# Kernel tuning notes

Measured on AMD Instinct MI355X. Metric: run time of the kernel, lower is better.

Reference implementation:

```python
import jax, jax.numpy as jnp
import numpy as np

D_MODEL = 1024
NUM_HEADS = 2
NUM_FEATURES = 256
DEPTH = D_MODEL // 2  # faithful to source: depth = d_model // 2
B, L = 4, 4096


def _orthogonal_gaussian(key, m, d):
    # Faithful port of orthogonal_gaussian: stacked QR blocks, scaled.
    num_squares = m // d
    remainder = m - d * num_squares
    keys = jax.random.split(key, num_squares + 1)
    blocks = []
    for i in range(num_squares):
        q, _ = jnp.linalg.qr(jax.random.normal(keys[i], (d, d)))
        blocks.append(q.T)
    if remainder:
        q, _ = jnp.linalg.qr(jax.random.normal(keys[-1], (d, d)))
        blocks.append(q.T[:remainder])
    mat = jnp.vstack(blocks)
    return mat / jnp.sqrt(jnp.float32(num_squares) + remainder / d)


def setup_inputs() -> dict:
    key = jax.random.key(0)
    ks = jax.random.split(key, 16)
    s = 0.02
    inp = {
        'query': jax.random.normal(ks[0], (B, L, D_MODEL), jnp.float32),
        'key':   jax.random.normal(ks[1], (B, L, D_MODEL), jnp.float32),
        'value': jax.random.normal(ks[2], (B, L, D_MODEL), jnp.float32),
        'mask':  jnp.zeros((B, 1, 1, L), jnp.float32),
        'Wq': jax.random.normal(ks[3], (D_MODEL, D_MODEL), jnp.float32) * s,
        'bq': jnp.zeros((D_MODEL,), jnp.float32),
        'Wk': jax.random.normal(ks[4], (D_MODEL, D_MODEL), jnp.float32) * s,
        'bk': jnp.zeros((D_MODEL,), jnp.float32),
        'Wv': jax.random.normal(ks[5], (D_MODEL, D_MODEL), jnp.float32) * s,
        'bv': jnp.zeros((D_MODEL,), jnp.float32),
        'Wo': jax.random.normal(ks[6], (D_MODEL, D_MODEL), jnp.float32) * s,
        'bo': jnp.zeros((D_MODEL,), jnp.float32),
        'random_feats': _orthogonal_gaussian(ks[7], NUM_FEATURES, DEPTH),
    }
    return inp


def _softmax_kernel(data, is_query, proj, eps=1e-6):
    # data: [B, L, H, D]; proj: [M, D]
    d = data.shape[-1]
    data = data * (1.0 / jnp.sqrt(jnp.sqrt(jnp.float32(d))))
    ratio = 1.0 / jnp.sqrt(jnp.float32(proj.shape[0]))
    data_dash = jnp.einsum('blhd,md->blhm', data, proj)  # [B,L,H,M]
    diag = jnp.sum(data * data, axis=-1, keepdims=True) * 0.5  # [B,L,H,1]
    if is_query:
        mx = jnp.max(data_dash, axis=-1, keepdims=True)
    else:
        # last_dims_t + attention_dims_t = (3, 1)
        mx = jnp.max(data_dash, axis=(3, 1), keepdims=True)
    return ratio * (jnp.exp(data_dash - diag - mx) + eps)


def _attn_hat(q, k, v, proj):
    # q,k,v: [B, H, Lh, D]  (Lh = 2L/num_heads from split_heads quirk)
    l = q.shape[0]  # faithful: tf.shape(query)[0] == batch
    q = jnp.transpose(q, (0, 2, 1, 3))  # [B, Lh, H, D]
    k = jnp.transpose(k, (0, 2, 1, 3))
    q_prime = _softmax_kernel(q, True, proj)   # [B, Lh, H, M]
    k_prime = _softmax_kernel(k, False, proj)
    v = jnp.transpose(v, (0, 2, 1, 3))         # [B, Lh, H, D]
    # Faithful einsums: axis0 labeled 'l' (=batch), axis1 labeled 'b' (=seq)
    av = jnp.einsum('lbhm,lbhd->bhmd', k_prime, v)
    av = jnp.einsum('lbhm,bhmd->lbhd', q_prime, av)
    norm = jnp.einsum('lbhm,l->bhm', k_prime, jnp.ones((l,), jnp.float32))
    norm = jnp.einsum('lbhm,bhm->lbh', q_prime, norm)
    av = jnp.transpose(av, (1, 0, 2, 3))       # [Lh, B, H, D]
    norm = jnp.transpose(norm, (1, 0, 2))[..., None]
    return av / norm


def reference(query, key, value, mask, Wq, bq, Wk, bk, Wv, bv, Wo, bo, random_feats):
    bsz = query.shape[0]
    q = query @ Wq + bq
    k = key @ Wk + bk
    v = value @ Wv + bv

    def split_heads(x):
        x = x.reshape(bsz, -1, NUM_HEADS, DEPTH)
        return jnp.transpose(x, (0, 2, 1, 3))

    q, k, v = split_heads(q), split_heads(k), split_heads(v)
    attn = _attn_hat(q, k, v, random_feats)        # [Lh, B, H, D]
    attn = jnp.transpose(attn, (0, 2, 1, 3))       # [Lh, H, B, D]
    concat = attn.reshape(bsz, -1, D_MODEL)
    return concat @ Wo + bo
```

## Files before the change

kernel.cpp:

```cpp
#include <hip/hip_runtime.h>
#include <cstdint>
#include <cstddef>

typedef unsigned short u16;
typedef __bf16 bf16x8 __attribute__((ext_vector_type(8)));
typedef unsigned short u16x8 __attribute__((ext_vector_type(8)));
typedef float   f32x4 __attribute__((ext_vector_type(4)));

#define D_MODEL 1024
#define NF      256
#define DEPTH   512
#define SEQ     4096
#define ROWS    16384
#define HROWS   32768

#define QK_SCALE      0.21022410381342864f
#define HALF_SCALE2   0.022097086912079608f

__device__ __forceinline__ u16 f2bf(float f) {
  union { float f; uint32_t u; } x; x.f = f;
  uint32_t r = x.u + 0x7FFFu + ((x.u >> 16) & 1u);
  return (u16)(r >> 16);
}
__device__ __forceinline__ float bf2f(u16 u) {
  union { uint32_t u; float f; } x; x.u = ((uint32_t)u) << 16;
  return x.f;
}

__device__ __forceinline__ void gload16(const u16* g, u16* l) {
  __builtin_amdgcn_global_load_lds((const __attribute__((address_space(1))) void*)g,
                                   (__attribute__((address_space(3))) void*)l,
                                   16, 0, 0);
}


__global__ void transpose4_kernel(const float* __restrict__ w0, const float* __restrict__ w1,
                                  const float* __restrict__ w2, const float* __restrict__ w3,
                                  u16* __restrict__ o0, u16* __restrict__ o1,
                                  u16* __restrict__ o2, u16* __restrict__ o3) {
  __shared__ float tile[32][33];
  int z = blockIdx.z;
  const float* src = (z == 0) ? w0 : (z == 1) ? w1 : (z == 2) ? w2 : w3;
  u16* dst         = (z == 0) ? o0 : (z == 1) ? o1 : (z == 2) ? o2 : o3;
  int bx = blockIdx.x * 32, by = blockIdx.y * 32;
  int tx = threadIdx.x, ty = threadIdx.y;
#pragma unroll
  for (int r = ty; r < 32; r += 8) tile[r][tx] = src[(size_t)(by + r) * D_MODEL + bx + tx];
  __syncthreads();
#pragma unroll
  for (int r = ty; r < 32; r += 8)
    dst[(size_t)(bx + r) * D_MODEL + by + tx] = f2bf(tile[tx][r]);
}

__global__ void projcvt_kernel(const float4* __restrict__ p, ushort4* __restrict__ o) {
  int i = blockIdx.x * 256 + threadIdx.x;
  float4 a = p[i];
  o[i] = make_ushort4(f2bf(a.x * QK_SCALE), f2bf(a.y * QK_SCALE),
                      f2bf(a.z * QK_SCALE), f2bf(a.w * QK_SCALE));
}

template <bool BF16OUT, bool AFP32>
__global__ __launch_bounds__(256) void gemm_bt_kernel(
    const void* __restrict__ Av, const u16* __restrict__ B, void* __restrict__ Cv,
    const float* __restrict__ bias, int K, int N) {
  __shared__ __align__(16) u16 As[128 * 32];
  __shared__ __align__(16) u16 Bs[128 * 32];
  const int tid  = threadIdx.x;
  const int lane = tid & 63;
  const int wave = tid >> 6;
  const int wm = wave >> 1, wn = wave & 1;
  const int quad = lane >> 4, l15 = lane & 15;
  const int bm = blockIdx.x, bn = blockIdx.y;
  const u16* Bb = (const u16*)B + (size_t)bn * 128 * K;

  const int srow = lane >> 2;
  const int scol = (lane & 3) * 8;
  const u16* Bg0 = Bb + (size_t)(wave * 32 + srow) * K + scol;
  const u16* Bg1 = Bg0 + (size_t)16 * K;
  u16* lA0 = As + wave * 1024;
  u16* lA1 = lA0 + 512;
  u16* lB0 = Bs + wave * 1024;
  u16* lB1 = lB0 + 512;

  const u16*   Ag0  = nullptr; const u16*   Ag1  = nullptr;
  const float* Af0  = nullptr; const float* Af1  = nullptr;
  if (AFP32) {
    const float* Ab = (const float*)Av + (size_t)bm * 128 * K;
    Af0 = Ab + (size_t)(wave * 32 + srow) * K + scol;
    Af1 = Af0 + (size_t)16 * K;
  } else {
    const u16* Ab = (const u16*)Av + (size_t)bm * 128 * K;
    Ag0 = Ab + (size_t)(wave * 32 + srow) * K + scol;
    Ag1 = Ag0 + (size_t)16 * K;
  }
  u16* wA0 = As + wave * 1024 + lane * 8;
  u16* wA1 = wA0 + 512;

  f32x4 acc[4][4] = {};

  for (int k0 = 0; k0 < K; k0 += 32) {
    __syncthreads();
    if (AFP32) {
      float4 p00 = *(const float4*)(Af0 + k0);
      float4 p01 = *(const float4*)(Af0 + k0 + 4);
      float4 p10 = *(const float4*)(Af1 + k0);
      float4 p11 = *(const float4*)(Af1 + k0 + 4);
      gload16(Bg0 + k0, lB0);
      gload16(Bg1 + k0, lB1);
      u16x8 c0, c1;
      c0[0]=f2bf(p00.x); c0[1]=f2bf(p00.y); c0[2]=f2bf(p00.z); c0[3]=f2bf(p00.w);
      c0[4]=f2bf(p01.x); c0[5]=f2bf(p01.y); c0[6]=f2bf(p01.z); c0[7]=f2bf(p01.w);
      c1[0]=f2bf(p10.x); c1[1]=f2bf(p10.y); c1[2]=f2bf(p10.z); c1[3]=f2bf(p10.w);
      c1[4]=f2bf(p11.x); c1[5]=f2bf(p11.y); c1[6]=f2bf(p11.z); c1[7]=f2bf(p11.w);
      *(u16x8*)wA0 = c0;
      *(u16x8*)wA1 = c1;
    } else {
      gload16(Ag0 + k0, lA0);
      gload16(Ag1 + k0, lA1);
      gload16(Bg0 + k0, lB0);
      gload16(Bg1 + k0, lB1);
    }
    __syncthreads();
    bf16x8 af[4], bfr[4];
#pragma unroll
    for (int mt = 0; mt < 4; mt++)
      af[mt] = *(const bf16x8*)&As[(wm * 64 + mt * 16 + l15) * 32 + quad * 8];
#pragma unroll
    for (int nt = 0; nt < 4; nt++)
      bfr[nt] = *(const bf16x8*)&Bs[(wn * 64 + nt * 16 + l15) * 32 + quad * 8];
#pragma unroll
    for (int mt = 0; mt < 4; mt++)
#pragma unroll
      for (int nt = 0; nt < 4; nt++)
        acc[mt][nt] = __builtin_amdgcn_mfma_f32_16x16x32_bf16(af[mt], bfr[nt], acc[mt][nt], 0, 0, 0);
  }

  const int rbase = bm * 128 + wm * 64 + quad * 4;
  const int cbase = bn * 128 + wn * 64 + l15;
#pragma unroll
  for (int nt = 0; nt < 4; nt++) {
    int col = cbase + nt * 16;
    float bvad = bias ? bias[col] : 0.0f;
#pragma unroll
    for (int mt = 0; mt < 4; mt++) {
#pragma unroll
      for (int r = 0; r < 4; r++) {
        int row = rbase + mt * 16 + r;
        float v = acc[mt][nt][r] + bvad;
        if (BF16OUT) ((u16*)Cv)[(size_t)row * N + col] = f2bf(v);
        else         ((float*)Cv)[(size_t)row * N + col] = v;
      }
    }
  }
}

__global__ void diag_kernel(const u16* __restrict__ Qb, const u16* __restrict__ Kb,
                            float* __restrict__ dq, float* __restrict__ dk) {
  const int wave = threadIdx.x >> 6, lane = threadIdx.x & 63;
  int row = blockIdx.x * 4 + wave;
  const u16* src; float* dst; int r;
  if (row < HROWS) { src = Qb; dst = dq; r = row; }
  else             { src = Kb; dst = dk; r = row - HROWS; }
  const ushort4* p = (const ushort4*)(src + (size_t)r * DEPTH);
  ushort4 u0 = p[lane * 2], u1 = p[lane * 2 + 1];
  float s = 0.f, f;
  f = bf2f(u0.x); s += f * f; f = bf2f(u0.y); s += f * f;
  f = bf2f(u0.z); s += f * f; f = bf2f(u0.w); s += f * f;
  f = bf2f(u1.x); s += f * f; f = bf2f(u1.y); s += f * f;
  f = bf2f(u1.z); s += f * f; f = bf2f(u1.w); s += f * f;
#pragma unroll
  for (int o = 32; o; o >>= 1) s += __shfl_xor(s, o);
  if (lane == 0) dst[r] = s * HALF_SCALE2;
}

__global__ void maxk_part_kernel(const float* __restrict__ kd, float* __restrict__ partials) {
  int g = blockIdx.x >> 6;
  int sb = blockIdx.x & 63;
  int b = g >> 1, h = g & 1;
  int tid = threadIdx.x;
  float mx = -3.4e38f;
  for (int j = 0; j < 64; j++) {
    int s = sb * 64 + j;
    int row = b * 8192 + s * 2 + h;
    mx = fmaxf(mx, kd[(size_t)row * NF + tid]);
  }
#pragma unroll
  for (int o = 32; o; o >>= 1) mx = fmaxf(mx, __shfl_xor(mx, o));
  __shared__ float wmax[4];
  if ((tid & 63) == 0) wmax[tid >> 6] = mx;
  __syncthreads();
  if (tid == 0)
    partials[blockIdx.x] = fmaxf(fmaxf(wmax[0], wmax[1]), fmaxf(wmax[2], wmax[3]));
}

__global__ void maxk_final_kernel(const float* __restrict__ partials, float* __restrict__ mxk) {
  float v = partials[blockIdx.x * 64 + threadIdx.x];
#pragma unroll
  for (int o = 32; o; o >>= 1) v = fmaxf(v, __shfl_xor(v, o));
  if (threadIdx.x == 0) mxk[blockIdx.x] = v;
}

__global__ __launch_bounds__(256) void attn_kernel(
    const float* __restrict__ qd, const float* __restrict__ kd,
    const float* __restrict__ diagq, const float* __restrict__ diagk,
    const float* __restrict__ mxk, const u16* __restrict__ Vb,
    u16* __restrict__ concat) {
  int s = blockIdx.x >> 1, h = blockIdx.x & 1;
  int t = threadIdx.x;
  int wave = t >> 6, lane = t & 63;
  __shared__ float qp[4][256], kp[4][256];
  __shared__ float As[4][4];
  __shared__ float wred[4][4];
  __shared__ float mqs[4];

  float qv[4], kv[4];
  int rows[4];
#pragma unroll
  for (int b = 0; b < 4; b++) {
    int r = b * 8192 + s * 2 + h;
    rows[b] = r;
    qv[b] = qd[(size_t)r * NF + t];
    kv[b] = kd[(size_t)r * NF + t];
  }
#pragma unroll
  for (int b = 0; b < 4; b++) {
    float v = qv[b];
#pragma unroll
    for (int o = 32; o; o >>= 1) v = fmaxf(v, __shfl_xor(v, o));
    if (lane == 0) wred[wave][b] = v;
  }
  __syncthreads();
  if (t < 4) mqs[t] = fmaxf(fmaxf(wred[0][t], wred[1][t]), fmaxf(wred[2][t], wred[3][t]));
  __syncthreads();
#pragma unroll
  for (int b = 0; b < 4; b++) {
    qp[b][t] = __expf(qv[b] - diagq[rows[b]] - mqs[b]) + 1e-6f;
    kp[b][t] = __expf(kv[b] - diagk[rows[b]] - mxk[b * 2 + h]) + 1e-6f;
  }
  __syncthreads();
  {
    int i = wave;
    float p0 = 0, p1 = 0, p2 = 0, p3 = 0;
    for (int m = lane; m < 256; m += 64) {
      float q = qp[i][m];
      p0 += q * kp[0][m]; p1 += q * kp[1][m];
      p2 += q * kp[2][m]; p3 += q * kp[3][m];
    }
#pragma unroll
    for (int o = 32; o; o >>= 1) {
      p0 += __shfl_xor(p0, o); p1 += __shfl_xor(p1, o);
      p2 += __shfl_xor(p2, o); p3 += __shfl_xor(p3, o);
    }
    if (lane == 0) { As[i][0] = p0; As[i][1] = p1; As[i][2] = p2; As[i][3] = p3; }
  }
  __syncthreads();
  float a00 = As[0][0], a01 = As[0][1], a02 = As[0][2], a03 = As[0][3];
  float a10 = As[1][0], a11 = As[1][1], a12 = As[1][2], a13 = As[1][3];
  float a20 = As[2][0], a21 = As[2][1], a22 = As[2][2], a23 = As[2][3];
  float a30 = As[3][0], a31 = As[3][1], a32 = As[3][2], a33 = As[3][3];
  float n0 = 1.f / (a00 + a01 + a02 + a03);
  float n1 = 1.f / (a10 + a11 + a12 + a13);
  float n2 = 1.f / (a20 + a21 + a22 + a23);
  float n3 = 1.f / (a30 + a31 + a32 + a33);
  size_t obase = (size_t)s * 4096 + (size_t)h * 2048;
#pragma unroll
  for (int dp = 0; dp < 2; dp++) {
    int d = t + dp * 256;
    float v0 = bf2f(Vb[((size_t)(0 * SEQ + s)) * D_MODEL + h * DEPTH + d]);
    float v1 = bf2f(Vb[((size_t)(1 * SEQ + s)) * D_MODEL + h * DEPTH + d]);
    float v2 = bf2f(Vb[((size_t)(2 * SEQ + s)) * D_MODEL + h * DEPTH + d]);
    float v3 = bf2f(Vb[((size_t)(3 * SEQ + s)) * D_MODEL + h * DEPTH + d]);
    concat[obase + 0 * 512 + d] = f2bf((a00 * v0 + a01 * v1 + a02 * v2 + a03 * v3) * n0);
    concat[obase + 1 * 512 + d] = f2bf((a10 * v0 + a11 * v1 + a12 * v2 + a13 * v3) * n1);
    concat[obase + 2 * 512 + d] = f2bf((a20 * v0 + a21 * v1 + a22 * v2 + a23 * v3) * n2);
    concat[obase + 3 * 512 + d] = f2bf((a30 * v0 + a31 * v1 + a32 * v2 + a33 * v3) * n3);
  }
}

extern "C" void kernel_launch(void* const* d_in, const int* in_sizes, int n_in,
                              void* d_out, int out_size, void* d_ws, size_t ws_size,
                              hipStream_t stream) {
  (void)in_sizes; (void)n_in; (void)out_size; (void)ws_size;
  const float* query = (const float*)d_in[0];
  const float* key   = (const float*)d_in[1];
  const float* value = (const float*)d_in[2];
  const float* Wq = (const float*)d_in[4];
  const float* bq = (const float*)d_in[5];
  const float* Wk = (const float*)d_in[6];
  const float* bk = (const float*)d_in[7];
  const float* Wv = (const float*)d_in[8];
  const float* bv = (const float*)d_in[9];
  const float* Wo = (const float*)d_in[10];
  const float* bo = (const float*)d_in[11];
  const float* proj = (const float*)d_in[12];
  float* out = (float*)d_out;

  char* w = (char*)d_ws;
  size_t o = 0;
  auto take = [&](size_t b) { void* p = w + o; o += (b + 255) & ~(size_t)255; return p; };
  u16* Wqt   = (u16*)take(2097152);
  u16* Wkt   = (u16*)take(2097152);
  u16* Wvt   = (u16*)take(2097152);
  u16* Wot   = (u16*)take(2097152);
  u16* projb = (u16*)take(262144);
  u16* Qb    = (u16*)take(33554432);
  u16* Kb    = (u16*)take(33554432);
  u16* Vb    = (u16*)take(33554432);
  float* qd  = (float*)take(33554432);
  float* kd  = (float*)take(33554432);
  u16* concat = (u16*)take(33554432);
  float* diagq    = (float*)take(131072);
  float* diagk    = (float*)take(131072);
  float* partials = (float*)take(2048);
  float* mxk      = (float*)take(64);

  transpose4_kernel<<<dim3(32, 32, 4), dim3(32, 8), 0, stream>>>(Wq, Wk, Wv, Wo,
                                                                 Wqt, Wkt, Wvt, Wot);
  projcvt_kernel<<<128, 256, 0, stream>>>((const float4*)proj, (ushort4*)projb);

  gemm_bt_kernel<true, true><<<dim3(128, 8), 256, 0, stream>>>(query, Wqt, Qb, bq, 1024, 1024);
  gemm_bt_kernel<true, true><<<dim3(128, 8), 256, 0, stream>>>(key,   Wkt, Kb, bk, 1024, 1024);
  gemm_bt_kernel<true, true><<<dim3(128, 8), 256, 0, stream>>>(value, Wvt, Vb, bv, 1024, 1024);

  diag_kernel<<<16384, 256, 0, stream>>>(Qb, Kb, diagq, diagk);

  gemm_bt_kernel<false, false><<<dim3(256, 2), 256, 0, stream>>>(Qb, projb, qd, nullptr, 512, 256);
  gemm_bt_kernel<false, false><<<dim3(256, 2), 256, 0, stream>>>(Kb, projb, kd, nullptr, 512, 256);

  maxk_part_kernel<<<512, 256, 0, stream>>>(kd, partials);
  maxk_final_kernel<<<8, 64, 0, stream>>>(partials, mxk);

  attn_kernel<<<8192, 256, 0, stream>>>(qd, kd, diagq, diagk, mxk, Vb, concat);

  gemm_bt_kernel<false, false><<<dim3(128, 8), 256, 0, stream>>>(concat, Wot, out, bo, 1024, 1024);
}
```

Measured before the change: 621.2 us.

## Double-buffer GEMM LDS tiles and swizzle chunks to avoid bank conflicts

The bf16 GEMM now holds two LDS buffers for A and B. The loads for the next K-slice are issued before the MFMAs on the current slice, so global memory latency can overlap compute. The 8-element column chunks are also rotated per row on both the write and the read side to cut LDS bank conflicts on the fragment reads. This doubles LDS use per block, which may lower occupancy. It also depends on the async global-to-LDS loads having finished by the barrier at the top of the next iteration.

```diff
diff --git a/kernel.cpp b/kernel.cpp
--- a/kernel.cpp
+++ b/kernel.cpp
@@ -63,27 +63,25 @@
 __global__ __launch_bounds__(256) void gemm_bt_kernel(
     const void* __restrict__ Av, const u16* __restrict__ B, void* __restrict__ Cv,
     const float* __restrict__ bias, int K, int N) {
-  __shared__ __align__(16) u16 As[128 * 32];
-  __shared__ __align__(16) u16 Bs[128 * 32];
+  __shared__ __align__(16) u16 As[2][128 * 32];
+  __shared__ __align__(16) u16 Bs[2][128 * 32];
   const int tid  = threadIdx.x;
   const int lane = tid & 63;
   const int wave = tid >> 6;
   const int wm = wave >> 1, wn = wave & 1;
   const int quad = lane >> 4, l15 = lane & 15;
   const int bm = blockIdx.x, bn = blockIdx.y;
-  const u16* Bb = (const u16*)B + (size_t)bn * 128 * K;
-
-  const int srow = lane >> 2;
-  const int scol = (lane & 3) * 8;
+
+  const int srow   = lane >> 2;
+  const int schunk = ((lane & 3) - (lane >> 3)) & 3;
+  const int scol   = schunk * 8;
+
+  const u16* Bb  = B + (size_t)bn * 128 * K;
   const u16* Bg0 = Bb + (size_t)(wave * 32 + srow) * K + scol;
   const u16* Bg1 = Bg0 + (size_t)16 * K;
-  u16* lA0 = As + wave * 1024;
-  u16* lA1 = lA0 + 512;
-  u16* lB0 = Bs + wave * 1024;
-  u16* lB1 = lB0 + 512;
-
-  const u16*   Ag0  = nullptr; const u16*   Ag1  = nullptr;
-  const float* Af0  = nullptr; const float* Af1  = nullptr;
+
+  const float* Af0 = nullptr; const float* Af1 = nullptr;
+  const u16*   Ag0 = nullptr; const u16*   Ag1 = nullptr;
   if (AFP32) {
     const float* Ab = (const float*)Av + (size_t)bm * 128 * K;
     Af0 = Ab + (size_t)(wave * 32 + srow) * K + scol;
@@ -93,41 +91,62 @@
     Ag0 = Ab + (size_t)(wave * 32 + srow) * K + scol;
     Ag1 = Ag0 + (size_t)16 * K;
   }
-  u16* wA0 = As + wave * 1024 + lane * 8;
-  u16* wA1 = wA0 + 512;
+
+  const int sslot0 = wave * 1024 + lane * 8;
+  const int sslot1 = sslot0 + 512;
+  const int ro = l15 * 32 + (((quad + (l15 >> 1)) & 3) * 8);
 
   f32x4 acc[4][4] = {};
+  float4 p00, p01, p10, p11;
+
+  if (AFP32) {
+    p00 = *(const float4*)(Af0);
+    p01 = *(const float4*)(Af0 + 4);
+    p10 = *(const float4*)(Af1);
+    p11 = *(const float4*)(Af1 + 4);
+  } else {
+    gload16(Ag0, &As[0][wave * 1024]);
+    gload16(Ag1, &As[0][wave * 1024 + 512]);
+  }
+  gload16(Bg0, &Bs[0][wave * 1024]);
+  gload16(Bg1, &Bs[0][wave * 1024 + 512]);
 
   for (int k0 = 0; k0 < K; k0 += 32) {
+    const int buf = (k0 >> 5) & 1;
+    const int nxt = buf ^ 1;
     __syncthreads();
     if (AFP32) {
-      float4 p00 = *(const float4*)(Af0 + k0);
-      float4 p01 = *(const float4*)(Af0 + k0 + 4);
-      float4 p10 = *(const float4*)(Af1 + k0);
-      float4 p11 = *(const float4*)(Af1 + k0 + 4);
-      gload16(Bg0 + k0, lB0);
-      gload16(Bg1 + k0, lB1);
       u16x8 c0, c1;
       c0[0]=f2bf(p00.x); c0[1]=f2bf(p00.y); c0[2]=f2bf(p00.z); c0[3]=f2bf(p00.w);
       c0[4]=f2bf(p01.x); c0[5]=f2bf(p01.y); c0[6]=f2bf(p01.z); c0[7]=f2bf(p01.w);
       c1[0]=f2bf(p10.x); c1[1]=f2bf(p10.y); c1[2]=f2bf(p10.z); c1[3]=f2bf(p10.w);
       c1[4]=f2bf(p11.x); c1[5]=f2bf(p11.y); c1[6]=f2bf(p11.z); c1[7]=f2bf(p11.w);
-      *(u16x8*)wA0 = c0;
-      *(u16x8*)wA1 = c1;
+      *(u16x8*)&As[buf][sslot0] = c0;
+      *(u16x8*)&As[buf][sslot1] = c1;
+      __syncthreads();
+      if (k0 + 32 < K) {
+        p00 = *(const float4*)(Af0 + k0 + 32);
+        p01 = *(const float4*)(Af0 + k0 + 36);
+        p10 = *(const float4*)(Af1 + k0 + 32);
+        p11 = *(const float4*)(Af1 + k0 + 36);
+        gload16(Bg0 + k0 + 32, &Bs[nxt][wave * 1024]);
+        gload16(Bg1 + k0 + 32, &Bs[nxt][wave * 1024 + 512]);
+      }
     } else {
-      gload16(Ag0 + k0, lA0);
-      gload16(Ag1 + k0, lA1);
-      gload16(Bg0 + k0, lB0);
-      gload16(Bg1 + k0, lB1);
+      if (k0 + 32 < K) {
+        gload16(Ag0 + k0 + 32, &As[nxt][wave * 1024]);
+        gload16(Ag1 + k0 + 32, &As[nxt][wave * 1024 + 512]);
+        gload16(Bg0 + k0 + 32, &Bs[nxt][wave * 1024]);
+        gload16(Bg1 + k0 + 32, &Bs[nxt][wave * 1024 + 512]);
+      }
     }
-    __syncthreads();
     bf16x8 af[4], bfr[4];
 #pragma unroll
     for (int mt = 0; mt < 4; mt++)
-      af[mt] = *(const bf16x8*)&As[(wm * 64 + mt * 16 + l15) * 32 + quad * 8];
+      af[mt] = *(const bf16x8*)&As[buf][(wm * 4 + mt) * 512 + ro];
 #pragma unroll
     for (int nt = 0; nt < 4; nt++)
-      bfr[nt] = *(const bf16x8*)&Bs[(wn * 64 + nt * 16 + l15) * 32 + quad * 8];
+      bfr[nt] = *(const bf16x8*)&Bs[buf][(wn * 4 + nt) * 512 + ro];
 #pragma unroll
     for (int mt = 0; mt < 4; mt++)
 #pragma unroll
```

Measured after the change: 593.8 us. 4.4% less time.
